# Kernel optimization log

Hardware: AMD Instinct MI355X
Metric: run time of the kernel (lower is better)

The kernel has to match this reference:

```python
import jax, jax.numpy as jnp
import numpy as np

C_IN, C_OUT = 256, 128

def setup_inputs() -> dict:
    key = jax.random.key(0)
    k1, k2, k3, k4, k5, k6 = jax.random.split(key, 6)
    B, H, W = 8, 64, 64
    p = jax.random.normal(k1, (B, C_IN, H, W), dtype=jnp.float32)
    b = jax.random.normal(k2, (B, C_IN, H, W), dtype=jnp.float32)
    # 1x1 conv weights (Conv2d with kernel 1 == pointwise matmul) + biases
    sq = 1.0 / np.sqrt(C_IN)
    Wq = jax.random.uniform(k3, (C_OUT, C_IN), jnp.float32, -sq, sq)
    bq = jax.random.uniform(k4, (C_OUT,), jnp.float32, -sq, sq)
    Wk = jax.random.uniform(k5, (C_OUT, C_IN), jnp.float32, -sq, sq)
    bk = jax.random.uniform(k6, (C_OUT,), jnp.float32, -sq, sq)
    return {"p": p, "b": b, "Wq": Wq, "bq": bq, "Wk": Wk, "bk": bk}

def reference(p, b, Wq, bq, Wk, bk):
    B, C, H, W = p.shape
    N = H * W
    # 1x1 convs -> flatten spatial dim to N
    q = jnp.einsum('bchw,oc->bhwo', p, Wq) + bq          # [B,H,W,Co]
    q = q.reshape(B, N, -1).astype(jnp.float32)           # [B,N,Co] (query permuted)
    k = jnp.einsum('bchw,oc->bohw', b, Wk) + bk[None, :, None, None]
    k = k.reshape(B, -1, N).astype(jnp.float32)           # [B,Co,N]
    energy = jnp.einsum('bnc,bcm->bnm', q, k)             # [B,N,N] unscaled
    attention = jax.nn.softmax(energy, axis=-1)           # softmax over keys
    value = b.reshape(B, C, N)                            # [B,C,N]
    out = jnp.einsum('bnm,bcm->bcn', attention, value)    # [B,C,N]
    return out.reshape(B, C, H, W)
```

## Files before the change

kernel.cpp:

```cpp
#include <hip/hip_runtime.h>
#include <hip/hip_bf16.h>
#include <math.h>


#define B_   8
#define CIN  256
#define COUT 128
#define NN   4096

typedef _Float16 half8  __attribute__((ext_vector_type(8)));
typedef short    short8 __attribute__((ext_vector_type(8)));
typedef float    f32x4  __attribute__((ext_vector_type(4)));

#define LOG2E 1.44269504088896340736f

__device__ __forceinline__ unsigned short f2h(float f) {
    union { _Float16 h; unsigned short u; } v; v.h = (_Float16)f;
    return v.u;
}
__device__ __forceinline__ unsigned int cvt_pk_bf16(float lo, float hi) {
    unsigned int r;
    asm("v_cvt_pk_bf16_f32 %0, %1, %2" : "=v"(r) : "v"(lo), "v"(hi));
    return r;
}
__device__ __forceinline__ unsigned int pkrtz(float lo, float hi) {
    typedef __fp16 fp16x2 __attribute__((ext_vector_type(2)));
    union { fp16x2 h; unsigned int u; } c;
    c.h = __builtin_amdgcn_cvt_pkrtz(lo, hi);
    return c.u;
}
__device__ __forceinline__ float dpp_xor1(float x) {
    union { float f; int i; } u; u.f = x;
    u.i = __builtin_amdgcn_mov_dpp(u.i, 0xB1, 0xF, 0xF, true);
    return u.f;
}
__device__ __forceinline__ void dma16(void* lds, const void* g) {
    __builtin_amdgcn_global_load_lds(
        (const __attribute__((address_space(1))) unsigned int*)g,
        (__attribute__((address_space(3))) unsigned int*)lds,
        16, 0, 0);
}

__global__ __launch_bounds__(256) void cvt_w(const float* __restrict__ Wq,
                                             const float* __restrict__ Wk,
                                             const float* __restrict__ bq,
                                             _Float16* __restrict__ Whq,
                                             _Float16* __restrict__ Whk,
                                             float* __restrict__ bqs) {
    const int bx = blockIdx.x, t = threadIdx.x;
    const int isK = (bx >= 32);
    const float* src = isK ? Wk : Wq;
    _Float16* dst = isK ? Whk : Whq;
    const float scale = isK ? 1.0f : LOG2E;
    const int idx = (bx & 31) * 256 + t;
    float4 v = ((const float4*)src)[idx];
    unsigned long long pk = (unsigned long long)f2h(v.x * scale)
                          | ((unsigned long long)f2h(v.y * scale) << 16)
                          | ((unsigned long long)f2h(v.z * scale) << 32)
                          | ((unsigned long long)f2h(v.w * scale) << 48);
    ((unsigned long long*)dst)[idx] = pk;
    if (bx == 0 && t < COUT) bqs[t] = bq[t] * LOG2E;
}

__global__ __launch_bounds__(256) void kv_prep(
        const float* __restrict__ Bv,
        const _Float16* __restrict__ Whk,
        const float* __restrict__ bk,
        _Float16* __restrict__ Ktt,
        unsigned short* __restrict__ Vb)
{
    __shared__ __align__(16) unsigned short T[64 * 136];
    const int bx = blockIdx.x;
    const int b  = bx >> 6, n0 = (bx & 63) << 6;
    const int t  = threadIdx.x;

    {
        const int cr = t >> 2;
        const int nch = (t & 3) << 4;
#pragma unroll
        for (int it = 0; it < 4; ++it) {
            const int c = it * 64 + cr;
            const float* src = Bv + ((size_t)(b * CIN + c) * NN + n0 + nch);
            unsigned int o2[8];
#pragma unroll
            for (int k = 0; k < 4; ++k) {
                float4 f = *(const float4*)(src + k * 4);
                o2[k * 2]     = cvt_pk_bf16(f.x, f.y);
                o2[k * 2 + 1] = cvt_pk_bf16(f.z, f.w);
            }
            unsigned short* dst = Vb + (size_t)(b * CIN + c) * NN + n0 + nch;
            *(int4*)dst = *(int4*)&o2[0];
            *(int4*)(dst + 8) = *(int4*)&o2[4];
        }
    }

    const int w = t >> 6, lane = t & 63, l15 = lane & 15, quad = lane >> 4, q8 = quad * 8;

    half8 a[8];
    {
        const float* Xa = Bv + ((size_t)(b * CIN + q8) * NN) + n0 + w * 16 + l15;
#pragma unroll
        for (int s = 0; s < 8; ++s) {
            const float* xs = Xa + (size_t)s * 32 * NN;
            float av[8];
#pragma unroll
            for (int j = 0; j < 8; ++j) av[j] = xs[(size_t)j * NN];
            union { half8 h; unsigned int u[4]; } af;
#pragma unroll
            for (int j = 0; j < 4; ++j) af.u[j] = pkrtz(av[2 * j], av[2 * j + 1]);
            a[s] = af.h;
        }
    }

    f32x4 D[8];
#pragma unroll
    for (int og = 0; og < 8; ++og) D[og] = (f32x4){0.f, 0.f, 0.f, 0.f};
    const _Float16* wbase = Whk + (size_t)l15 * CIN + q8;
#pragma unroll
    for (int s = 0; s < 8; ++s) {
        const _Float16* wp = wbase + s * 32;
#pragma unroll
        for (int og = 0; og < 8; ++og) {
            half8 wfv = *(const half8*)(wp + og * 16 * CIN);
            D[og] = __builtin_amdgcn_mfma_f32_16x16x32_f16(a[s], wfv, D[og], 0, 0, 0);
        }
    }

    const int nrow = w * 16 + quad * 4;
#pragma unroll
    for (int og = 0; og < 8; ++og) {
        const int o = og * 16 + l15;
        const float bo = bk[o];
        const int c = o >> 3, j = o & 7;
        const int sw = (c & 7) << 2;
#pragma unroll
        for (int r2 = 0; r2 < 4; ++r2) {
            const int n = nrow + r2;
            const int tl = n >> 5, m = n & 31;
            T[tl * 4096 + (c * 32 + ((m + sw) & 31)) * 8 + j] = f2h(D[og][r2] + bo);
        }
    }
    __syncthreads();
    _Float16* dstk = Ktt + ((size_t)(b * 128 + (n0 >> 5)) * 4096 + t * 32);
    const unsigned short* srck = T + t * 32;
#pragma unroll
    for (int k = 0; k < 4; ++k)
        ((int4*)dstk)[k] = ((const int4*)srck)[k];
}

__global__ __launch_bounds__(256, 2) void flash_kernel(const float* __restrict__ Pin,
                                                       const _Float16* __restrict__ Whq,
                                                       const float* __restrict__ bqs,
                                                       const _Float16* __restrict__ Ktt,
                                                       const unsigned short* __restrict__ V,
                                                       float* __restrict__ out) {
    __shared__ __align__(16) char SH[76032];
    _Float16*       K0sh = (_Float16*)(SH);
    _Float16*       K1sh = (_Float16*)(SH + 8192);
    unsigned short* V0sh = (unsigned short*)(SH + 16384);
    unsigned short* V1sh = (unsigned short*)(SH + 32768);
    unsigned short* V2sh = (unsigned short*)(SH + 49152);
    unsigned short* P0sh = (unsigned short*)(SH + 65536);
    unsigned short* P1sh = (unsigned short*)(SH + 70656);
    float*          Lsh  = (float*)(SH + 75776);
    unsigned short* T    = (unsigned short*)SH;

    const int bx   = blockIdx.x;
    const int b    = bx >> 6;
    const int q0   = (bx & 63) << 6;
    const int t    = threadIdx.x;
    const int w    = t >> 6;
    const int lane = t & 63;
    const int l15  = lane & 15;
    const int quad = lane >> 4;
    const int q8   = quad * 8;

    const _Float16* Kb = Ktt + (size_t)b * 128 * 4096;
    const unsigned short* Vg = V + (size_t)b * CIN * NN;

    half8 Qf[4];
    {
        half8 a[8];
        const float* Xa = Pin + ((size_t)(b * CIN + q8) * NN) + q0 + w * 16 + l15;
#pragma unroll
        for (int s = 0; s < 8; ++s) {
            const float* xs = Xa + (size_t)s * 32 * NN;
            float av[8];
#pragma unroll
            for (int j = 0; j < 8; ++j) av[j] = xs[(size_t)j * NN];
            union { half8 h; unsigned int u[4]; } af;
#pragma unroll
            for (int j = 0; j < 4; ++j) af.u[j] = pkrtz(av[2 * j], av[2 * j + 1]);
            a[s] = af.h;
        }
        f32x4 D[8];
#pragma unroll
        for (int og = 0; og < 8; ++og) D[og] = (f32x4){0.f, 0.f, 0.f, 0.f};
        const _Float16* wbase = Whq + (size_t)l15 * CIN + q8;
#pragma unroll
        for (int s = 0; s < 8; ++s) {
            const _Float16* wp = wbase + s * 32;
#pragma unroll
            for (int og = 0; og < 8; ++og) {
                half8 wfv = *(const half8*)(wp + og * 16 * CIN);
                D[og] = __builtin_amdgcn_mfma_f32_16x16x32_f16(a[s], wfv, D[og], 0, 0, 0);
            }
        }
        const int nrow = w * 16 + quad * 4;
#pragma unroll
        for (int og = 0; og < 8; ++og) {
            const int o = og * 16 + l15;
            const float bo = bqs[o];
#pragma unroll
            for (int r2 = 0; r2 < 4; ++r2)
                T[(nrow + r2) * 136 + o] = f2h(D[og][r2] + bo);
        }
        __syncthreads();
#pragma unroll
        for (int s = 0; s < 4; ++s)
            Qf[s] = *(const half8*)&T[(w * 16 + l15) * 136 + s * 32 + q8];
        __syncthreads();
    }

    f32x4 O[16];
#pragma unroll
    for (int i = 0; i < 16; ++i) O[i] = (f32x4){0.f, 0.f, 0.f, 0.f};
    float lsum[4] = {0.f, 0.f, 0.f, 0.f};

    const int vmq   = ((lane & 3) - ((lane >> 3) & 3)) & 3;
    const int vcrow = lane >> 2;
    const int vslot = (quad + (l15 >> 1)) & 3;

    auto issueK = [&](int kt, _Float16* Kd) {
        const _Float16* gk = Kb + (size_t)kt * 4096;
        dma16(Kd + (w * 2 + 0) * 512, gk + (w * 2 + 0) * 512 + lane * 8);
        dma16(Kd + (w * 2 + 1) * 512, gk + (w * 2 + 1) * 512 + lane * 8);
    };
    auto issueV = [&](int kt, unsigned short* Vd) {
        const int k0 = kt << 5;
#pragma unroll
        for (int i = 0; i < 4; ++i) {
            const int cc = (w * 4 + i) * 16 + vcrow;
            dma16(Vd + (w * 4 + i) * 512,
                  Vg + (size_t)cc * NN + k0 + vmq * 8);
        }
    };

    auto halfstep = [&](int kt, const _Float16* Kc, _Float16* Kn,
                        const unsigned short* Va, unsigned short* Vn2,
                        unsigned short* Pc) {
        if (kt + 1 < 128) issueK(kt + 1, Kn);

        f32x4 S0 = {0.f, 0.f, 0.f, 0.f}, S1 = {0.f, 0.f, 0.f, 0.f};
        __builtin_amdgcn_s_setprio(1);
#pragma unroll
        for (int s = 0; s < 4; ++s) {
            const int kc = 4 * s + quad;
            const int sw = (kc & 7) << 2;
            const int x0 = (l15 + sw) & 31;
            half8 kf0 = *(const half8*)(Kc + (kc * 32 + x0) * 8);
            half8 kf1 = *(const half8*)(Kc + (kc * 32 + (x0 ^ 16)) * 8);
            S0 = __builtin_amdgcn_mfma_f32_16x16x32_f16(Qf[s], kf0, S0, 0, 0, 0);
            S1 = __builtin_amdgcn_mfma_f32_16x16x32_f16(Qf[s], kf1, S1, 0, 0, 0);
        }
        __builtin_amdgcn_s_setprio(0);

        f32x4 E0, E1;
#pragma unroll
        for (int r = 0; r < 4; ++r) {
            E0[r] = exp2f(S0[r]);
            E1[r] = exp2f(S1[r]);
            lsum[r] += E0[r] + E1[r];
        }
        {
            f32x4 P0, P1;
#pragma unroll
            for (int r = 0; r < 4; ++r) { P0[r] = dpp_xor1(E0[r]); P1[r] = dpp_xor1(E1[r]); }
            const int odd = l15 & 1;
            unsigned short* wp0 = Pc + w * 640
                                + (((quad << 2) + (odd << 1)) * 40) + (l15 & ~1);
            unsigned int pk0 = cvt_pk_bf16(odd ? P0[2] : E0[0], odd ? E0[2] : P0[0]);
            unsigned int pk1 = cvt_pk_bf16(odd ? P0[3] : E0[1], odd ? E0[3] : P0[1]);
            unsigned int pk2 = cvt_pk_bf16(odd ? P1[2] : E1[0], odd ? E1[2] : P1[0]);
            unsigned int pk3 = cvt_pk_bf16(odd ? P1[3] : E1[1], odd ? E1[3] : P1[1]);
            *(unsigned int*)&wp0[0]  = pk0;
            *(unsigned int*)&wp0[40] = pk1;
            *(unsigned int*)&wp0[16] = pk2;
            *(unsigned int*)&wp0[56] = pk3;
        }

        __syncthreads();

        if (kt + 2 < 128) issueV(kt + 2, Vn2);

        {
            short8 pf[4];
#pragma unroll
            for (int ni = 0; ni < 4; ++ni)
                pf[ni] = *(const short8*)(Pc + (ni * 16 + l15) * 40 + q8);
            const unsigned short* vb = Va + (w * 64 + l15) * 32 + vslot * 8;
            __builtin_amdgcn_s_setprio(1);
#pragma unroll
            for (int cj = 0; cj < 4; ++cj) {
                short8 vf = *(const short8*)(vb + cj * 512);
#pragma unroll
                for (int ni = 0; ni < 4; ++ni)
                    O[ni * 4 + cj] = __builtin_amdgcn_mfma_f32_16x16x32_bf16(pf[ni], vf, O[ni * 4 + cj], 0, 0, 0);
            }
            __builtin_amdgcn_s_setprio(0);
        }
    };

    issueK(0, K0sh);
    issueV(0, V0sh);
    issueV(1, V1sh);
    __syncthreads();

    _Float16*       Kc = K0sh; _Float16*       Kn = K1sh;
    unsigned short* Va = V0sh; unsigned short* Vm = V1sh; unsigned short* Vn2 = V2sh;
    unsigned short* Pc = P0sh; unsigned short* Pn = P1sh;
#pragma unroll 1
    for (int kt = 0; kt < 128; ++kt) {
        halfstep(kt, Kc, Kn, Va, Vn2, Pc);
        _Float16* tk = Kc; Kc = Kn; Kn = tk;
        unsigned short* tv = Va; Va = Vm; Vm = Vn2; Vn2 = tv;
        unsigned short* tp = Pc; Pc = Pn; Pn = tp;
    }

#pragma unroll
    for (int r = 0; r < 4; ++r) {
        float s = lsum[r];
        s += __shfl_xor(s, 1);
        s += __shfl_xor(s, 2);
        s += __shfl_xor(s, 4);
        s += __shfl_xor(s, 8);
        if (l15 == 0) Lsh[w * 16 + (quad << 2) + r] = s;
    }
    __syncthreads();
    float* ob = out + (size_t)b * CIN * NN + q0;
#pragma unroll
    for (int ni = 0; ni < 4; ++ni) {
        const f32x4 lv = *(const f32x4*)&Lsh[ni * 16 + (quad << 2)];
        f32x4 linv;
#pragma unroll
        for (int r = 0; r < 4; ++r) linv[r] = 1.0f / lv[r];
        const int nb = ni * 16 + (quad << 2);
#pragma unroll
        for (int cj = 0; cj < 4; ++cj) {
            const int c = w * 64 + cj * 16 + l15;
            f32x4 val = O[ni * 4 + cj];
#pragma unroll
            for (int r = 0; r < 4; ++r) val[r] *= linv[r];
            *(f32x4*)(ob + (size_t)c * NN + nb) = val;
        }
    }
}

extern "C" void kernel_launch(void* const* d_in, const int* in_sizes, int n_in,
                              void* d_out, int out_size, void* d_ws, size_t ws_size,
                              hipStream_t stream) {
    const float* p  = (const float*)d_in[0];
    const float* bv = (const float*)d_in[1];
    const float* Wq = (const float*)d_in[2];
    const float* bq = (const float*)d_in[3];
    const float* Wk = (const float*)d_in[4];
    const float* bk = (const float*)d_in[5];
    float* outp = (float*)d_out;

    char* ws = (char*)d_ws;
    const size_t szK = (size_t)B_ * NN * COUT * 2;
    const size_t szV = (size_t)B_ * NN * CIN * 2;
    const size_t szW = (size_t)COUT * CIN * 2;
    _Float16*       Ktt = (_Float16*)ws;
    unsigned short* Vb  = (unsigned short*)(ws + szK);
    _Float16*       Whq = (_Float16*)(ws + szK + szV);
    _Float16*       Whk = (_Float16*)(ws + szK + szV + szW);
    float*          bqs = (float*)(ws + szK + szV + 2 * szW);

    cvt_w<<<64, 256, 0, stream>>>(Wq, Wk, bq, Whq, Whk, bqs);
    kv_prep<<<512, 256, 0, stream>>>(bv, Whk, bk, Ktt, Vb);
    flash_kernel<<<512, 256, 0, stream>>>(p, Whq, bqs, Ktt, Vb, outp);
}
```

Baseline: 275.8 us.

## Load V fragments directly into registers and shrink LDS for higher occupancy

V tiles are no longer staged through a triple-buffered shared-memory DMA ring. Each lane now loads its bf16 V fragments straight from global memory into registers, two tiles ahead. This frees about 49 KB of LDS, and the launch bound is raised to 4 blocks per CU to hide latency with more occupancy. The risks are register pressure from 4-block occupancy plus the extra V registers, and uncoalesced 16-byte global loads from strided rows, each row being NN apart.

```diff
diff --git a/kernel.cpp b/kernel.cpp
--- a/kernel.cpp
+++ b/kernel.cpp
@@ -148,21 +148,18 @@
         ((int4*)dstk)[k] = ((const int4*)srck)[k];
 }
 
-__global__ __launch_bounds__(256, 2) void flash_kernel(const float* __restrict__ Pin,
+__global__ __launch_bounds__(256, 4) void flash_kernel(const float* __restrict__ Pin,
                                                        const _Float16* __restrict__ Whq,
                                                        const float* __restrict__ bqs,
                                                        const _Float16* __restrict__ Ktt,
                                                        const unsigned short* __restrict__ V,
                                                        float* __restrict__ out) {
-    __shared__ __align__(16) char SH[76032];
+    __shared__ __align__(16) char SH[27136];
     _Float16*       K0sh = (_Float16*)(SH);
     _Float16*       K1sh = (_Float16*)(SH + 8192);
-    unsigned short* V0sh = (unsigned short*)(SH + 16384);
-    unsigned short* V1sh = (unsigned short*)(SH + 32768);
-    unsigned short* V2sh = (unsigned short*)(SH + 49152);
-    unsigned short* P0sh = (unsigned short*)(SH + 65536);
-    unsigned short* P1sh = (unsigned short*)(SH + 70656);
-    float*          Lsh  = (float*)(SH + 75776);
+    unsigned short* P0sh = (unsigned short*)(SH + 16384);
+    unsigned short* P1sh = (unsigned short*)(SH + 21504);
+    float*          Lsh  = (float*)(SH + 26624);
     unsigned short* T    = (unsigned short*)SH;
 
     const int bx   = blockIdx.x;
@@ -227,28 +224,22 @@
     for (int i = 0; i < 16; ++i) O[i] = (f32x4){0.f, 0.f, 0.f, 0.f};
     float lsum[4] = {0.f, 0.f, 0.f, 0.f};
 
-    const int vmq   = ((lane & 3) - ((lane >> 3) & 3)) & 3;
-    const int vcrow = lane >> 2;
-    const int vslot = (quad + (l15 >> 1)) & 3;
+    const unsigned short* Vlane = Vg + (size_t)(w * 64 + l15) * NN + q8;
+    short8 VA[4], VB[4];
 
     auto issueK = [&](int kt, _Float16* Kd) {
         const _Float16* gk = Kb + (size_t)kt * 4096;
         dma16(Kd + (w * 2 + 0) * 512, gk + (w * 2 + 0) * 512 + lane * 8);
         dma16(Kd + (w * 2 + 1) * 512, gk + (w * 2 + 1) * 512 + lane * 8);
     };
-    auto issueV = [&](int kt, unsigned short* Vd) {
-        const int k0 = kt << 5;
-#pragma unroll
-        for (int i = 0; i < 4; ++i) {
-            const int cc = (w * 4 + i) * 16 + vcrow;
-            dma16(Vd + (w * 4 + i) * 512,
-                  Vg + (size_t)cc * NN + k0 + vmq * 8);
-        }
+    auto loadV = [&](int kt, short8* Vd) {
+#pragma unroll
+        for (int cj = 0; cj < 4; ++cj)
+            Vd[cj] = *(const short8*)(Vlane + (size_t)cj * 16 * NN + kt * 32);
     };
 
     auto halfstep = [&](int kt, const _Float16* Kc, _Float16* Kn,
-                        const unsigned short* Va, unsigned short* Vn2,
-                        unsigned short* Pc) {
+                        unsigned short* Pc, short8* Vcur) {
         if (kt + 1 < 128) issueK(kt + 1, Kn);
 
         f32x4 S0 = {0.f, 0.f, 0.f, 0.f}, S1 = {0.f, 0.f, 0.f, 0.f};
@@ -291,40 +282,33 @@
 
         __syncthreads();
 
-        if (kt + 2 < 128) issueV(kt + 2, Vn2);
-
         {
             short8 pf[4];
 #pragma unroll
             for (int ni = 0; ni < 4; ++ni)
                 pf[ni] = *(const short8*)(Pc + (ni * 16 + l15) * 40 + q8);
-            const unsigned short* vb = Va + (w * 64 + l15) * 32 + vslot * 8;
             __builtin_amdgcn_s_setprio(1);
 #pragma unroll
             for (int cj = 0; cj < 4; ++cj) {
-                short8 vf = *(const short8*)(vb + cj * 512);
+                short8 vf = Vcur[cj];
 #pragma unroll
                 for (int ni = 0; ni < 4; ++ni)
                     O[ni * 4 + cj] = __builtin_amdgcn_mfma_f32_16x16x32_bf16(pf[ni], vf, O[ni * 4 + cj], 0, 0, 0);
             }
             __builtin_amdgcn_s_setprio(0);
         }
+        if (kt + 2 < 128) loadV(kt + 2, Vcur);
     };
 
     issueK(0, K0sh);
-    issueV(0, V0sh);
-    issueV(1, V1sh);
+    loadV(0, VA);
+    loadV(1, VB);
     __syncthreads();
 
-    _Float16*       Kc = K0sh; _Float16*       Kn = K1sh;
-    unsigned short* Va = V0sh; unsigned short* Vm = V1sh; unsigned short* Vn2 = V2sh;
-    unsigned short* Pc = P0sh; unsigned short* Pn = P1sh;
 #pragma unroll 1
-    for (int kt = 0; kt < 128; ++kt) {
-        halfstep(kt, Kc, Kn, Va, Vn2, Pc);
-        _Float16* tk = Kc; Kc = Kn; Kn = tk;
-        unsigned short* tv = Va; Va = Vm; Vm = Vn2; Vn2 = tv;
-        unsigned short* tp = Pc; Pc = Pn; Pn = tp;
+    for (int kt = 0; kt < 128; kt += 2) {
+        halfstep(kt,     K0sh, K1sh, P0sh, VA);
+        halfstep(kt + 1, K1sh, K0sh, P1sh, VB);
     }
 
 #pragma unroll
```

Measured after the change: 638.5 us. +131.5%, slower.
